# Kernel optimization log

Measured on AMD Instinct MI355X. Metric: run time of the kernel, lower is better.

The kernel has to match this reference:

```python
import jax, jax.numpy as jnp
import numpy as np

N_NODES = 100000
N_EDGES = 1250000
D_FEAT = 64


def setup_inputs() -> dict:
    key = jax.random.key(0)
    kx, ke = jax.random.split(key)
    x = jax.random.normal(kx, (N_NODES, D_FEAT), dtype=jnp.float32)
    edge_index = jax.random.randint(ke, (2, N_EDGES), 0, N_NODES, dtype=jnp.int64)
    return {"x": x, "edge_index": edge_index}


def reference(x, edge_index):
    # propagate: scatter_nested gathers x[idxj] grouped by destination idxi
    # (a ragged per-node neighbor set); the module's sum_nested reduces each
    # group. Expressed densely and jit-ably as gather + segment-sum.
    idxi = edge_index[0, :]  # destination nodes
    idxj = edge_index[1, :]  # source nodes
    messages = x[idxj]  # [E, D] edge-level gather (memory-bound)
    out = jax.ops.segment_sum(messages, idxi, num_segments=N_NODES)  # [N, D]
    return out
```

## Files before the change

kernel.cpp:

```cpp
#include <hip/hip_runtime.h>

#define N_NODES 100000
#define N_EDGES 1250000
#define D_FEAT  64

#define NPB     256
#define NBINS   ((N_NODES + NPB - 1) / NPB)
#define BCAP    4096
#define EPB     4096
#define K1B     ((N_EDGES + EPB - 1) / EPB)
#define OVF_CAP 32768

#define CAP     48


__global__ __launch_bounds__(512) void k1_bin_kernel(
        const int* __restrict__ idxi, const int* __restrict__ idxj,
        int* __restrict__ gcursor, int* __restrict__ ovfcnt,
        int* __restrict__ ovf, int* __restrict__ binbuf) {
    __shared__ int hist[512];
    __shared__ int runstart[512];
    __shared__ int gbase[NBINS];
    __shared__ int cur[NBINS];
    __shared__ int staged[EPB];
    __shared__ unsigned short sbin[EPB];
    int t = threadIdx.x;
    hist[t] = 0;
    __syncthreads();

    long long base = (long long)blockIdx.x * EPB;
    int d[8], s[8], bn[8];
#pragma unroll
    for (int j = 0; j < 8; ++j) {
        long long e = base + t + j * 512;
        if (e < N_EDGES) {
            d[j] = idxi[e];
            s[j] = idxj[e];
            bn[j] = d[j] >> 8;
            atomicAdd(&hist[bn[j]], 1);
        } else {
            bn[j] = -1;
        }
    }
    __syncthreads();

    runstart[t] = hist[t];
    __syncthreads();
    for (int off = 1; off < 512; off <<= 1) {
        int add = (t >= off) ? runstart[t - off] : 0;
        __syncthreads();
        runstart[t] += add;
        __syncthreads();
    }
    int excl = runstart[t] - hist[t];
    __syncthreads();
    runstart[t] = excl;
    if (t < NBINS) {
        gbase[t] = hist[t] ? atomicAdd(&gcursor[t], hist[t]) : 0;
        cur[t] = 0;
    }
    __syncthreads();

#pragma unroll
    for (int j = 0; j < 8; ++j) {
        if (bn[j] >= 0) {
            int lofs = atomicAdd(&cur[bn[j]], 1);
            int idx = runstart[bn[j]] + lofs;
            staged[idx] = ((d[j] & 255) << 17) | s[j];
            sbin[idx] = (unsigned short)bn[j];
        }
    }
    __syncthreads();

    long long rem = (long long)N_EDGES - base;
    int n = (rem < EPB) ? (int)rem : EPB;
    for (int i = t; i < n; i += 512) {
        int b = sbin[i];
        int p = staged[i];
        int tgt = gbase[b] + (i - runstart[b]);
        if (tgt < BCAP) {
            binbuf[(size_t)b * BCAP + tgt] = p;
        } else {
            int op = atomicAdd(ovfcnt, 1);
            if (op < OVF_CAP) { ovf[2 * op] = b * NPB + (p >> 17); ovf[2 * op + 1] = p & 0x1FFFF; }
        }
    }
}

__global__ __launch_bounds__(1024) void k23_fused_kernel(
        const float* __restrict__ x, const int* __restrict__ gcursor,
        const int* __restrict__ binbuf, float* __restrict__ out) {
    __shared__ int cnt[NPB];
    __shared__ int excl[NPB];
    __shared__ int cur[NPB];
    __shared__ int stmp[NPB];
    __shared__ int srt[BCAP];
    int bin = blockIdx.x;
    int t = threadIdx.x;
    if (t < NPB) cnt[t] = 0;
    __syncthreads();

    int n = gcursor[bin];
    if (n > BCAP) n = BCAP;
    const int* src = binbuf + (size_t)bin * BCAP;
    int p[4];
#pragma unroll
    for (int j = 0; j < 4; ++j) {
        int i = t + j * 1024;
        p[j] = (i < n) ? src[i] : -1;
        if (p[j] >= 0) atomicAdd(&cnt[p[j] >> 17], 1);
    }
    __syncthreads();

    if (t < NPB) stmp[t] = cnt[t];
    __syncthreads();
    for (int off = 1; off < NPB; off <<= 1) {
        int v = 0;
        if (t < NPB && t >= off) v = stmp[t - off];
        __syncthreads();
        if (t < NPB) stmp[t] += v;
        __syncthreads();
    }
    if (t < NPB) {
        excl[t] = stmp[t] - cnt[t];
        cur[t] = 0;
    }
    __syncthreads();

#pragma unroll
    for (int j = 0; j < 4; ++j) {
        if (p[j] >= 0) {
            int dl = p[j] >> 17;
            int pos = excl[dl] + atomicAdd(&cur[dl], 1);
            srt[pos] = p[j] & 0x1FFFF;
        }
    }
    __syncthreads();

    int wave = t >> 6;
    int lane = t & 63;
    int sub  = lane >> 4;
    int c4   = lane & 15;
    for (int i = 0; i < 16; ++i) {
        int dloc = wave * 16 + i;
        int node = bin * NPB + dloc;
        if (node >= N_NODES) break;
        int base = excl[dloc];
        int l = cnt[dloc];
        float4 acc = make_float4(0.f, 0.f, 0.f, 0.f);
        int k = 0;
        for (; k + 8 <= l; k += 8) {
            int s0 = srt[base + k + sub];
            int s1 = srt[base + k + 4 + sub];
            const float4 v0 = *(const float4*)(x + (size_t)s0 * D_FEAT + c4 * 4);
            const float4 v1 = *(const float4*)(x + (size_t)s1 * D_FEAT + c4 * 4);
            acc.x += v0.x + v1.x;
            acc.y += v0.y + v1.y;
            acc.z += v0.z + v1.z;
            acc.w += v0.w + v1.w;
        }
        if (k + 4 <= l) {
            int s0 = srt[base + k + sub];
            const float4 v0 = *(const float4*)(x + (size_t)s0 * D_FEAT + c4 * 4);
            acc.x += v0.x; acc.y += v0.y; acc.z += v0.z; acc.w += v0.w;
            k += 4;
        }
        if (k + sub < l) {
            int s0 = srt[base + k + sub];
            const float4 v0 = *(const float4*)(x + (size_t)s0 * D_FEAT + c4 * 4);
            acc.x += v0.x; acc.y += v0.y; acc.z += v0.z; acc.w += v0.w;
        }

        acc.x += __shfl_xor(acc.x, 16, 64);
        acc.y += __shfl_xor(acc.y, 16, 64);
        acc.z += __shfl_xor(acc.z, 16, 64);
        acc.w += __shfl_xor(acc.w, 16, 64);
        acc.x += __shfl_xor(acc.x, 32, 64);
        acc.y += __shfl_xor(acc.y, 32, 64);
        acc.z += __shfl_xor(acc.z, 32, 64);
        acc.w += __shfl_xor(acc.w, 32, 64);

        if (lane < 16) {
            ((float4*)out)[(size_t)node * 16 + c4] = acc;
        }
    }
}

__global__ __launch_bounds__(256) void ovf_fixup_kernel(
        const float* __restrict__ x, const int* __restrict__ ovfcnt,
        const int* __restrict__ ovf, float* __restrict__ out) {
    int n = *ovfcnt;
    if (n > OVF_CAP) n = OVF_CAP;
    long long total = (long long)n * 16;
    long long stride = (long long)gridDim.x * blockDim.x;
    for (long long t = blockIdx.x * blockDim.x + threadIdx.x; t < total; t += stride) {
        int e  = (int)(t >> 4);
        int fo = ((int)t & 15) << 2;
        int d = ovf[2 * e];
        int s = ovf[2 * e + 1];
        const float4 v = *(const float4*)(x + (size_t)s * D_FEAT + fo);
        float* o = out + (size_t)d * D_FEAT + fo;
        atomicAdd(o + 0, v.x);
        atomicAdd(o + 1, v.y);
        atomicAdd(o + 2, v.z);
        atomicAdd(o + 3, v.w);
    }
}


__global__ __launch_bounds__(256) void scatter_pad_kernel(
        const int* __restrict__ idxi, const int* __restrict__ idxj,
        int* __restrict__ cnt, int* __restrict__ ovfcnt,
        int* __restrict__ ovf, int* __restrict__ bucket) {
    int e = blockIdx.x * blockDim.x + threadIdx.x;
    if (e >= N_EDGES) return;
    int d = idxi[e];
    int s = idxj[e];
    int pos = atomicAdd(&cnt[d], 1);
    if (pos < CAP) {
        bucket[(size_t)d * CAP + pos] = s;
    } else {
        int op = atomicAdd(ovfcnt, 1);
        if (op < OVF_CAP) { ovf[2 * op] = d; ovf[2 * op + 1] = s; }
    }
}

__global__ __launch_bounds__(256) void gather_pad_kernel(
        const float* __restrict__ x, const int* __restrict__ cnt,
        const int* __restrict__ bucket, float* __restrict__ out) {
    int node = blockIdx.x * 4 + (threadIdx.x >> 6);
    int lane = threadIdx.x & 63;
    if (node >= N_NODES) return;
    int c = cnt[node];
    if (c > CAP) c = CAP;
    const int* b = bucket + (size_t)node * CAP;
    float acc = 0.f;
    int k = 0;
    for (; k + 4 <= c; k += 4) {
        int4 s4 = *(const int4*)(b + k);
        float a0 = x[(size_t)s4.x * D_FEAT + lane];
        float a1 = x[(size_t)s4.y * D_FEAT + lane];
        float a2 = x[(size_t)s4.z * D_FEAT + lane];
        float a3 = x[(size_t)s4.w * D_FEAT + lane];
        acc += (a0 + a1) + (a2 + a3);
    }
    for (; k < c; ++k) acc += x[(size_t)b[k] * D_FEAT + lane];
    out[(size_t)node * D_FEAT + lane] = acc;
}


__global__ __launch_bounds__(256) void zero_f4_kernel(float* __restrict__ out, int n4) {
    int i = blockIdx.x * blockDim.x + threadIdx.x;
    if (i < n4) ((float4*)out)[i] = make_float4(0.f, 0.f, 0.f, 0.f);
}

__global__ __launch_bounds__(256) void scatter_add_kernel(const float* __restrict__ x,
                                                          const int* __restrict__ idxi,
                                                          const int* __restrict__ idxj,
                                                          float* __restrict__ out) {
    int t = blockIdx.x * blockDim.x + threadIdx.x;
    int e = t >> 4;
    if (e >= N_EDGES) return;
    int fo = (t & 15) << 2;
    int dst = idxi[e];
    int src = idxj[e];
    const float4 v = *(const float4*)(x + (size_t)src * D_FEAT + fo);
    float* o = out + (size_t)dst * D_FEAT + fo;
    atomicAdd(o + 0, v.x);
    atomicAdd(o + 1, v.y);
    atomicAdd(o + 2, v.z);
    atomicAdd(o + 3, v.w);
}

extern "C" void kernel_launch(void* const* d_in, const int* in_sizes, int n_in,
                              void* d_out, int out_size, void* d_ws, size_t ws_size,
                              hipStream_t stream) {
    const float* x  = (const float*)d_in[0];
    const int*   ei = (const int*)d_in[1];
    const int*   idxi = ei;
    const int*   idxj = ei + N_EDGES;
    float* out = (float*)d_out;

    int nbe = (N_EDGES + 255) / 256;
    int gather_blocks = (N_NODES + 3) / 4;

    {
        size_t need = (512 + 16 + 2 * (size_t)OVF_CAP +
                       (size_t)NBINS * BCAP) * sizeof(int);
        if (ws_size >= need) {
            int* gcursor = (int*)d_ws;
            int* ovfcnt  = gcursor + 512;
            int* ovf     = ovfcnt + 16;
            int* binbuf  = ovf + 2 * OVF_CAP;

            hipMemsetAsync(gcursor, 0, (512 + 16) * sizeof(int), stream);
            k1_bin_kernel<<<K1B, 512, 0, stream>>>(idxi, idxj, gcursor, ovfcnt, ovf, binbuf);
            k23_fused_kernel<<<NBINS, 1024, 0, stream>>>(x, gcursor, binbuf, out);
            ovf_fixup_kernel<<<16, 256, 0, stream>>>(x, ovfcnt, ovf, out);
            return;
        }
    }

    {
        size_t need = ((size_t)N_NODES + 16 + 2 * (size_t)OVF_CAP +
                       (size_t)N_NODES * CAP) * sizeof(int);
        if (ws_size >= need) {
            int* cnt    = (int*)d_ws;
            int* ovfcnt = cnt + N_NODES;
            int* ovf    = cnt + N_NODES + 16;
            int* bucket = ovf + 2 * OVF_CAP;

            hipMemsetAsync(cnt, 0, (N_NODES + 16) * sizeof(int), stream);
            scatter_pad_kernel<<<nbe, 256, 0, stream>>>(idxi, idxj, cnt, ovfcnt, ovf, bucket);
            gather_pad_kernel<<<gather_blocks, 256, 0, stream>>>(x, cnt, bucket, out);
            ovf_fixup_kernel<<<16, 256, 0, stream>>>(x, ovfcnt, ovf, out);
            return;
        }
    }

    int n4 = (N_NODES * D_FEAT) / 4;
    zero_f4_kernel<<<(n4 + 255) / 256, 256, 0, stream>>>(out, n4);
    long long total_threads = (long long)N_EDGES * 16;
    scatter_add_kernel<<<(int)((total_threads + 255) / 256), 256, 0, stream>>>(x, idxi, idxj, out);
}
```

Measured before the change: 140.8 us.

## Fuse binning and per-bin gather into one cooperative persistent kernel

Replaces the memset plus three-kernel pipeline (bin, fused sort/gather, overflow fixup) with a single cooperative kernel of 256 blocks of 1024 threads. It zeroes the cursors, bins edges by destination, and after a grid sync sorts each bin locally and gathers with float4 loads plus a wave-level shuffle reduction. Overflow edges are folded in by a linear scan per node instead of a separate atomic kernel. This aims to remove launch and inter-kernel gaps. The costs are grid-sync overhead, lower parallelism (256 blocks walk 391 bins), and a per-node overflow scan that could be expensive if overflow is non-empty.

```diff
diff --git a/kernel.cpp b/kernel.cpp
--- a/kernel.cpp
+++ b/kernel.cpp
@@ -1,4 +1,7 @@
 #include <hip/hip_runtime.h>
+#include <hip/hip_cooperative_groups.h>
+
+namespace cg = cooperative_groups;
 
 #define N_NODES 100000
 #define N_EDGES 1250000
@@ -7,11 +10,216 @@
 #define NPB     256
 #define NBINS   ((N_NODES + NPB - 1) / NPB)
 #define BCAP    4096
+#define GRID    256
+#define EPB_A   ((N_EDGES + GRID - 1) / GRID)
+#define EPAD    4896
+#define OVF_CAP 32768
+
+#define CAP     48
 #define EPB     4096
 #define K1B     ((N_EDGES + EPB - 1) / EPB)
-#define OVF_CAP 32768
-
-#define CAP     48
+
+
+__global__ __launch_bounds__(1024) void mega_kernel(
+        const float* __restrict__ x,
+        const int* __restrict__ idxi, const int* __restrict__ idxj,
+        int* __restrict__ gcursor, int* __restrict__ ovfcnt,
+        int* __restrict__ ovf, int* __restrict__ binbuf,
+        float* __restrict__ out) {
+    __shared__ union {
+        struct {
+            int hist[512];
+            int runstart[512];
+            int gbase[NBINS];
+            int curA[NBINS];
+            int staged[EPAD];
+            unsigned short sbin[EPAD];
+        } a;
+        struct {
+            int cnt[NPB];
+            int excl[NPB];
+            int cur[NPB];
+            int stmp[NPB];
+            int srt[BCAP];
+        } b;
+    } sh;
+
+    cg::grid_group grid = cg::this_grid();
+    int t = threadIdx.x;
+    int gtid = blockIdx.x * 1024 + t;
+
+    if (gtid < NBINS) gcursor[gtid] = 0;
+    if (gtid == NBINS) *ovfcnt = 0;
+    grid.sync();
+
+    int base = blockIdx.x * EPB_A;
+    int end  = base + EPB_A;
+    if (end > N_EDGES) end = N_EDGES;
+
+    if (t < 512) sh.a.hist[t] = 0;
+    __syncthreads();
+
+    int d[5], s[5], bn[5];
+#pragma unroll
+    for (int j = 0; j < 5; ++j) {
+        int e = base + t + j * 1024;
+        if (e < end) {
+            d[j] = idxi[e];
+            s[j] = idxj[e];
+            bn[j] = d[j] >> 8;
+            atomicAdd(&sh.a.hist[bn[j]], 1);
+        } else {
+            bn[j] = -1;
+        }
+    }
+    __syncthreads();
+
+    if (t < 512) sh.a.runstart[t] = sh.a.hist[t];
+    __syncthreads();
+    for (int off = 1; off < 512; off <<= 1) {
+        int add = 0;
+        if (t < 512 && t >= off) add = sh.a.runstart[t - off];
+        __syncthreads();
+        if (t < 512) sh.a.runstart[t] += add;
+        __syncthreads();
+    }
+    int excl = 0;
+    if (t < 512) excl = sh.a.runstart[t] - sh.a.hist[t];
+    __syncthreads();
+    if (t < 512) sh.a.runstart[t] = excl;
+    if (t < NBINS) {
+        sh.a.gbase[t] = sh.a.hist[t] ? atomicAdd(&gcursor[t], sh.a.hist[t]) : 0;
+        sh.a.curA[t] = 0;
+    }
+    __syncthreads();
+
+#pragma unroll
+    for (int j = 0; j < 5; ++j) {
+        if (bn[j] >= 0) {
+            int lofs = atomicAdd(&sh.a.curA[bn[j]], 1);
+            int idx = sh.a.runstart[bn[j]] + lofs;
+            sh.a.staged[idx] = ((d[j] & 255) << 17) | s[j];
+            sh.a.sbin[idx] = (unsigned short)bn[j];
+        }
+    }
+    __syncthreads();
+
+    int n = end - base;
+    for (int i = t; i < n; i += 1024) {
+        int b = sh.a.sbin[i];
+        int p = sh.a.staged[i];
+        int tgt = sh.a.gbase[b] + (i - sh.a.runstart[b]);
+        if (tgt < BCAP) {
+            binbuf[(size_t)b * BCAP + tgt] = p;
+        } else {
+            int op = atomicAdd(ovfcnt, 1);
+            if (op < OVF_CAP) { ovf[2 * op] = b * NPB + (p >> 17); ovf[2 * op + 1] = p & 0x1FFFF; }
+        }
+    }
+
+    grid.sync();
+
+    int novf = *ovfcnt;
+    if (novf > OVF_CAP) novf = OVF_CAP;
+
+    for (int bin = blockIdx.x; bin < NBINS; bin += GRID) {
+        __syncthreads();
+        if (t < NPB) sh.b.cnt[t] = 0;
+        __syncthreads();
+
+        int nb = gcursor[bin];
+        if (nb > BCAP) nb = BCAP;
+        const int* src = binbuf + (size_t)bin * BCAP;
+        int p[4];
+#pragma unroll
+        for (int j = 0; j < 4; ++j) {
+            int i = t + j * 1024;
+            p[j] = (i < nb) ? src[i] : -1;
+            if (p[j] >= 0) atomicAdd(&sh.b.cnt[p[j] >> 17], 1);
+        }
+        __syncthreads();
+
+        if (t < NPB) sh.b.stmp[t] = sh.b.cnt[t];
+        __syncthreads();
+        for (int off = 1; off < NPB; off <<= 1) {
+            int v = 0;
+            if (t < NPB && t >= off) v = sh.b.stmp[t - off];
+            __syncthreads();
+            if (t < NPB) sh.b.stmp[t] += v;
+            __syncthreads();
+        }
+        if (t < NPB) {
+            sh.b.excl[t] = sh.b.stmp[t] - sh.b.cnt[t];
+            sh.b.cur[t] = 0;
+        }
+        __syncthreads();
+
+#pragma unroll
+        for (int j = 0; j < 4; ++j) {
+            if (p[j] >= 0) {
+                int dl = p[j] >> 17;
+                int pos = sh.b.excl[dl] + atomicAdd(&sh.b.cur[dl], 1);
+                sh.b.srt[pos] = p[j] & 0x1FFFF;
+            }
+        }
+        __syncthreads();
+
+        int wave = t >> 6;
+        int lane = t & 63;
+        int sub  = lane >> 4;
+        int c4   = lane & 15;
+        for (int i = 0; i < 16; ++i) {
+            int dloc = wave * 16 + i;
+            int node = bin * NPB + dloc;
+            if (node >= N_NODES) break;
+            int lbase = sh.b.excl[dloc];
+            int l = sh.b.cnt[dloc];
+            float4 acc = make_float4(0.f, 0.f, 0.f, 0.f);
+            int k = 0;
+            for (; k + 8 <= l; k += 8) {
+                int s0 = sh.b.srt[lbase + k + sub];
+                int s1 = sh.b.srt[lbase + k + 4 + sub];
+                const float4 v0 = *(const float4*)(x + (size_t)s0 * D_FEAT + c4 * 4);
+                const float4 v1 = *(const float4*)(x + (size_t)s1 * D_FEAT + c4 * 4);
+                acc.x += v0.x + v1.x;
+                acc.y += v0.y + v1.y;
+                acc.z += v0.z + v1.z;
+                acc.w += v0.w + v1.w;
+            }
+            if (k + 4 <= l) {
+                int s0 = sh.b.srt[lbase + k + sub];
+                const float4 v0 = *(const float4*)(x + (size_t)s0 * D_FEAT + c4 * 4);
+                acc.x += v0.x; acc.y += v0.y; acc.z += v0.z; acc.w += v0.w;
+                k += 4;
+            }
+            if (k + sub < l) {
+                int s0 = sh.b.srt[lbase + k + sub];
+                const float4 v0 = *(const float4*)(x + (size_t)s0 * D_FEAT + c4 * 4);
+                acc.x += v0.x; acc.y += v0.y; acc.z += v0.z; acc.w += v0.w;
+            }
+
+            acc.x += __shfl_xor(acc.x, 16, 64);
+            acc.y += __shfl_xor(acc.y, 16, 64);
+            acc.z += __shfl_xor(acc.z, 16, 64);
+            acc.w += __shfl_xor(acc.w, 16, 64);
+            acc.x += __shfl_xor(acc.x, 32, 64);
+            acc.y += __shfl_xor(acc.y, 32, 64);
+            acc.z += __shfl_xor(acc.z, 32, 64);
+            acc.w += __shfl_xor(acc.w, 32, 64);
+
+            if (lane < 16) {
+                for (int o = 0; o < novf; ++o) {
+                    if (ovf[2 * o] == node) {
+                        int ss = ovf[2 * o + 1];
+                        const float4 vv = *(const float4*)(x + (size_t)ss * D_FEAT + c4 * 4);
+                        acc.x += vv.x; acc.y += vv.y; acc.z += vv.z; acc.w += vv.w;
+                    }
+                }
+                ((float4*)out)[(size_t)node * 16 + c4] = acc;
+            }
+        }
+    }
+}
 
 
 __global__ __launch_bounds__(512) void k1_bin_kernel(
@@ -208,47 +416,6 @@
 }
 
 
-__global__ __launch_bounds__(256) void scatter_pad_kernel(
-        const int* __restrict__ idxi, const int* __restrict__ idxj,
-        int* __restrict__ cnt, int* __restrict__ ovfcnt,
-        int* __restrict__ ovf, int* __restrict__ bucket) {
-    int e = blockIdx.x * blockDim.x + threadIdx.x;
-    if (e >= N_EDGES) return;
-    int d = idxi[e];
-    int s = idxj[e];
-    int pos = atomicAdd(&cnt[d], 1);
-    if (pos < CAP) {
-        bucket[(size_t)d * CAP + pos] = s;
-    } else {
-        int op = atomicAdd(ovfcnt, 1);
-        if (op < OVF_CAP) { ovf[2 * op] = d; ovf[2 * op + 1] = s; }
-    }
-}
-
-__global__ __launch_bounds__(256) void gather_pad_kernel(
-        const float* __restrict__ x, const int* __restrict__ cnt,
-        const int* __restrict__ bucket, float* __restrict__ out) {
-    int node = blockIdx.x * 4 + (threadIdx.x >> 6);
-    int lane = threadIdx.x & 63;
-    if (node >= N_NODES) return;
-    int c = cnt[node];
-    if (c > CAP) c = CAP;
-    const int* b = bucket + (size_t)node * CAP;
-    float acc = 0.f;
-    int k = 0;
-    for (; k + 4 <= c; k += 4) {
-        int4 s4 = *(const int4*)(b + k);
-        float a0 = x[(size_t)s4.x * D_FEAT + lane];
-        float a1 = x[(size_t)s4.y * D_FEAT + lane];
-        float a2 = x[(size_t)s4.z * D_FEAT + lane];
-        float a3 = x[(size_t)s4.w * D_FEAT + lane];
-        acc += (a0 + a1) + (a2 + a3);
-    }
-    for (; k < c; ++k) acc += x[(size_t)b[k] * D_FEAT + lane];
-    out[(size_t)node * D_FEAT + lane] = acc;
-}
-
-
 __global__ __launch_bounds__(256) void zero_f4_kernel(float* __restrict__ out, int n4) {
     int i = blockIdx.x * blockDim.x + threadIdx.x;
     if (i < n4) ((float4*)out)[i] = make_float4(0.f, 0.f, 0.f, 0.f);
@@ -281,41 +448,26 @@
     const int*   idxj = ei + N_EDGES;
     float* out = (float*)d_out;
 
-    int nbe = (N_EDGES + 255) / 256;
-    int gather_blocks = (N_NODES + 3) / 4;
-
-    {
-        size_t need = (512 + 16 + 2 * (size_t)OVF_CAP +
-                       (size_t)NBINS * BCAP) * sizeof(int);
-        if (ws_size >= need) {
-            int* gcursor = (int*)d_ws;
-            int* ovfcnt  = gcursor + 512;
-            int* ovf     = ovfcnt + 16;
-            int* binbuf  = ovf + 2 * OVF_CAP;
-
-            hipMemsetAsync(gcursor, 0, (512 + 16) * sizeof(int), stream);
-            k1_bin_kernel<<<K1B, 512, 0, stream>>>(idxi, idxj, gcursor, ovfcnt, ovf, binbuf);
-            k23_fused_kernel<<<NBINS, 1024, 0, stream>>>(x, gcursor, binbuf, out);
-            ovf_fixup_kernel<<<16, 256, 0, stream>>>(x, ovfcnt, ovf, out);
-            return;
-        }
-    }
-
-    {
-        size_t need = ((size_t)N_NODES + 16 + 2 * (size_t)OVF_CAP +
-                       (size_t)N_NODES * CAP) * sizeof(int);
-        if (ws_size >= need) {
-            int* cnt    = (int*)d_ws;
-            int* ovfcnt = cnt + N_NODES;
-            int* ovf    = cnt + N_NODES + 16;
-            int* bucket = ovf + 2 * OVF_CAP;
-
-            hipMemsetAsync(cnt, 0, (N_NODES + 16) * sizeof(int), stream);
-            scatter_pad_kernel<<<nbe, 256, 0, stream>>>(idxi, idxj, cnt, ovfcnt, ovf, bucket);
-            gather_pad_kernel<<<gather_blocks, 256, 0, stream>>>(x, cnt, bucket, out);
-            ovf_fixup_kernel<<<16, 256, 0, stream>>>(x, ovfcnt, ovf, out);
-            return;
-        }
+    size_t need = (512 + 16 + 2 * (size_t)OVF_CAP +
+                   (size_t)NBINS * BCAP) * sizeof(int);
+    if (ws_size >= need) {
+        int* gcursor = (int*)d_ws;
+        int* ovfcnt  = gcursor + 512;
+        int* ovf     = ovfcnt + 16;
+        int* binbuf  = ovf + 2 * OVF_CAP;
+
+        void* args[] = { (void*)&x, (void*)&idxi, (void*)&idxj,
+                         (void*)&gcursor, (void*)&ovfcnt, (void*)&ovf,
+                         (void*)&binbuf, (void*)&out };
+        hipError_t err = hipLaunchCooperativeKernel(
+            (const void*)mega_kernel, dim3(GRID), dim3(1024), args, 0, stream);
+        if (err == hipSuccess) return;
+
+        hipMemsetAsync(gcursor, 0, (512 + 16) * sizeof(int), stream);
+        k1_bin_kernel<<<K1B, 512, 0, stream>>>(idxi, idxj, gcursor, ovfcnt, ovf, binbuf);
+        k23_fused_kernel<<<NBINS, 1024, 0, stream>>>(x, gcursor, binbuf, out);
+        ovf_fixup_kernel<<<16, 256, 0, stream>>>(x, ovfcnt, ovf, out);
+        return;
     }
 
     int n4 = (N_NODES * D_FEAT) / 4;
```

Measured after the change: 207.4 us. 47.3% more time.

## Gather from fp16 copy of node features in fused bin kernel

Applied to the files above, without the earlier changes.

Adds a conversion kernel that writes x as fp16 into the workspace, and a variant of the fused sort-and-gather kernel that reads fp16 rows with ushort4 loads and accumulates in fp32. Four edges are processed in parallel per wave, with shuffle reductions across 16-lane groups. The goal is to halve the bytes of the random row gathers, which dominate the kernel, at the cost of an extra pass over x and reduced input precision. The padded-bucket fallback path is removed.

```diff
diff --git a/kernel.cpp b/kernel.cpp
--- a/kernel.cpp
+++ b/kernel.cpp
@@ -1,4 +1,5 @@
 #include <hip/hip_runtime.h>
+#include <hip/hip_fp16.h>
 
 #define N_NODES 100000
 #define N_EDGES 1250000
@@ -11,8 +12,19 @@
 #define K1B     ((N_EDGES + EPB - 1) / EPB)
 #define OVF_CAP 32768
 
-#define CAP     48
-
+
+__global__ __launch_bounds__(256) void cvt_kernel(const float* __restrict__ x,
+                                                  unsigned short* __restrict__ xh) {
+    int i = blockIdx.x * 256 + threadIdx.x;
+    if (i >= N_NODES * D_FEAT / 4) return;
+    const float4 v = ((const float4*)x)[i];
+    ushort4 h;
+    h.x = __half_as_ushort(__float2half_rn(v.x));
+    h.y = __half_as_ushort(__float2half_rn(v.y));
+    h.z = __half_as_ushort(__float2half_rn(v.z));
+    h.w = __half_as_ushort(__float2half_rn(v.w));
+    ((ushort4*)xh)[i] = h;
+}
 
 __global__ __launch_bounds__(512) void k1_bin_kernel(
         const int* __restrict__ idxi, const int* __restrict__ idxj,
@@ -83,6 +95,111 @@
         } else {
             int op = atomicAdd(ovfcnt, 1);
             if (op < OVF_CAP) { ovf[2 * op] = b * NPB + (p >> 17); ovf[2 * op + 1] = p & 0x1FFFF; }
+        }
+    }
+}
+
+__global__ __launch_bounds__(1024) void k23_fused_h_kernel(
+        const unsigned short* __restrict__ xh, const int* __restrict__ gcursor,
+        const int* __restrict__ binbuf, float* __restrict__ out) {
+    __shared__ int cnt[NPB];
+    __shared__ int excl[NPB];
+    __shared__ int cur[NPB];
+    __shared__ int stmp[NPB];
+    __shared__ int srt[BCAP];
+    int bin = blockIdx.x;
+    int t = threadIdx.x;
+    if (t < NPB) cnt[t] = 0;
+    __syncthreads();
+
+    int n = gcursor[bin];
+    if (n > BCAP) n = BCAP;
+    const int* src = binbuf + (size_t)bin * BCAP;
+    int p[4];
+#pragma unroll
+    for (int j = 0; j < 4; ++j) {
+        int i = t + j * 1024;
+        p[j] = (i < n) ? src[i] : -1;
+        if (p[j] >= 0) atomicAdd(&cnt[p[j] >> 17], 1);
+    }
+    __syncthreads();
+
+    if (t < NPB) stmp[t] = cnt[t];
+    __syncthreads();
+    for (int off = 1; off < NPB; off <<= 1) {
+        int v = 0;
+        if (t < NPB && t >= off) v = stmp[t - off];
+        __syncthreads();
+        if (t < NPB) stmp[t] += v;
+        __syncthreads();
+    }
+    if (t < NPB) {
+        excl[t] = stmp[t] - cnt[t];
+        cur[t] = 0;
+    }
+    __syncthreads();
+
+#pragma unroll
+    for (int j = 0; j < 4; ++j) {
+        if (p[j] >= 0) {
+            int dl = p[j] >> 17;
+            int pos = excl[dl] + atomicAdd(&cur[dl], 1);
+            srt[pos] = p[j] & 0x1FFFF;
+        }
+    }
+    __syncthreads();
+
+    int wave = t >> 6;
+    int lane = t & 63;
+    int sub  = lane >> 4;
+    int c4   = lane & 15;
+    for (int i = 0; i < 16; ++i) {
+        int dloc = wave * 16 + i;
+        int node = bin * NPB + dloc;
+        if (node >= N_NODES) break;
+        int base = excl[dloc];
+        int l = cnt[dloc];
+        float4 acc = make_float4(0.f, 0.f, 0.f, 0.f);
+        int k = 0;
+        for (; k + 8 <= l; k += 8) {
+            int s0 = srt[base + k + sub];
+            int s1 = srt[base + k + 4 + sub];
+            ushort4 r0 = ((const ushort4*)(xh + (size_t)s0 * D_FEAT))[c4];
+            ushort4 r1 = ((const ushort4*)(xh + (size_t)s1 * D_FEAT))[c4];
+            acc.x += __half2float(__ushort_as_half(r0.x)) + __half2float(__ushort_as_half(r1.x));
+            acc.y += __half2float(__ushort_as_half(r0.y)) + __half2float(__ushort_as_half(r1.y));
+            acc.z += __half2float(__ushort_as_half(r0.z)) + __half2float(__ushort_as_half(r1.z));
+            acc.w += __half2float(__ushort_as_half(r0.w)) + __half2float(__ushort_as_half(r1.w));
+        }
+        if (k + 4 <= l) {
+            int s0 = srt[base + k + sub];
+            ushort4 r0 = ((const ushort4*)(xh + (size_t)s0 * D_FEAT))[c4];
+            acc.x += __half2float(__ushort_as_half(r0.x));
+            acc.y += __half2float(__ushort_as_half(r0.y));
+            acc.z += __half2float(__ushort_as_half(r0.z));
+            acc.w += __half2float(__ushort_as_half(r0.w));
+            k += 4;
+        }
+        if (k + sub < l) {
+            int s0 = srt[base + k + sub];
+            ushort4 r0 = ((const ushort4*)(xh + (size_t)s0 * D_FEAT))[c4];
+            acc.x += __half2float(__ushort_as_half(r0.x));
+            acc.y += __half2float(__ushort_as_half(r0.y));
+            acc.z += __half2float(__ushort_as_half(r0.z));
+            acc.w += __half2float(__ushort_as_half(r0.w));
+        }
+
+        acc.x += __shfl_xor(acc.x, 16, 64);
+        acc.y += __shfl_xor(acc.y, 16, 64);
+        acc.z += __shfl_xor(acc.z, 16, 64);
+        acc.w += __shfl_xor(acc.w, 16, 64);
+        acc.x += __shfl_xor(acc.x, 32, 64);
+        acc.y += __shfl_xor(acc.y, 32, 64);
+        acc.z += __shfl_xor(acc.z, 32, 64);
+        acc.w += __shfl_xor(acc.w, 32, 64);
+
+        if (lane < 16) {
+            ((float4*)out)[(size_t)node * 16 + c4] = acc;
         }
     }
 }
@@ -208,47 +325,6 @@
 }
 
 
-__global__ __launch_bounds__(256) void scatter_pad_kernel(
-        const int* __restrict__ idxi, const int* __restrict__ idxj,
-        int* __restrict__ cnt, int* __restrict__ ovfcnt,
-        int* __restrict__ ovf, int* __restrict__ bucket) {
-    int e = blockIdx.x * blockDim.x + threadIdx.x;
-    if (e >= N_EDGES) return;
-    int d = idxi[e];
-    int s = idxj[e];
-    int pos = atomicAdd(&cnt[d], 1);
-    if (pos < CAP) {
-        bucket[(size_t)d * CAP + pos] = s;
-    } else {
-        int op = atomicAdd(ovfcnt, 1);
-        if (op < OVF_CAP) { ovf[2 * op] = d; ovf[2 * op + 1] = s; }
-    }
-}
-
-__global__ __launch_bounds__(256) void gather_pad_kernel(
-        const float* __restrict__ x, const int* __restrict__ cnt,
-        const int* __restrict__ bucket, float* __restrict__ out) {
-    int node = blockIdx.x * 4 + (threadIdx.x >> 6);
-    int lane = threadIdx.x & 63;
-    if (node >= N_NODES) return;
-    int c = cnt[node];
-    if (c > CAP) c = CAP;
-    const int* b = bucket + (size_t)node * CAP;
-    float acc = 0.f;
-    int k = 0;
-    for (; k + 4 <= c; k += 4) {
-        int4 s4 = *(const int4*)(b + k);
-        float a0 = x[(size_t)s4.x * D_FEAT + lane];
-        float a1 = x[(size_t)s4.y * D_FEAT + lane];
-        float a2 = x[(size_t)s4.z * D_FEAT + lane];
-        float a3 = x[(size_t)s4.w * D_FEAT + lane];
-        acc += (a0 + a1) + (a2 + a3);
-    }
-    for (; k < c; ++k) acc += x[(size_t)b[k] * D_FEAT + lane];
-    out[(size_t)node * D_FEAT + lane] = acc;
-}
-
-
 __global__ __launch_bounds__(256) void zero_f4_kernel(float* __restrict__ out, int n4) {
     int i = blockIdx.x * blockDim.x + threadIdx.x;
     if (i < n4) ((float4*)out)[i] = make_float4(0.f, 0.f, 0.f, 0.f);
@@ -281,41 +357,30 @@
     const int*   idxj = ei + N_EDGES;
     float* out = (float*)d_out;
 
-    int nbe = (N_EDGES + 255) / 256;
-    int gather_blocks = (N_NODES + 3) / 4;
-
-    {
-        size_t need = (512 + 16 + 2 * (size_t)OVF_CAP +
-                       (size_t)NBINS * BCAP) * sizeof(int);
-        if (ws_size >= need) {
-            int* gcursor = (int*)d_ws;
-            int* ovfcnt  = gcursor + 512;
-            int* ovf     = ovfcnt + 16;
-            int* binbuf  = ovf + 2 * OVF_CAP;
-
-            hipMemsetAsync(gcursor, 0, (512 + 16) * sizeof(int), stream);
-            k1_bin_kernel<<<K1B, 512, 0, stream>>>(idxi, idxj, gcursor, ovfcnt, ovf, binbuf);
+    size_t base_ints = 512 + 16 + 2 * (size_t)OVF_CAP + (size_t)NBINS * BCAP;
+    size_t xh_ints   = (size_t)N_NODES * D_FEAT / 2;
+    size_t need_h    = (base_ints + xh_ints) * sizeof(int);
+    size_t need_f    = base_ints * sizeof(int);
+
+    if (ws_size >= need_f) {
+        int* gcursor = (int*)d_ws;
+        int* ovfcnt  = gcursor + 512;
+        int* ovf     = ovfcnt + 16;
+        int* binbuf  = ovf + 2 * OVF_CAP;
+
+        hipMemsetAsync(gcursor, 0, (512 + 16) * sizeof(int), stream);
+        k1_bin_kernel<<<K1B, 512, 0, stream>>>(idxi, idxj, gcursor, ovfcnt, ovf, binbuf);
+
+        if (ws_size >= need_h) {
+            unsigned short* xh = (unsigned short*)(binbuf + (size_t)NBINS * BCAP);
+            int n4 = N_NODES * D_FEAT / 4;
+            cvt_kernel<<<(n4 + 255) / 256, 256, 0, stream>>>(x, xh);
+            k23_fused_h_kernel<<<NBINS, 1024, 0, stream>>>(xh, gcursor, binbuf, out);
+        } else {
             k23_fused_kernel<<<NBINS, 1024, 0, stream>>>(x, gcursor, binbuf, out);
-            ovf_fixup_kernel<<<16, 256, 0, stream>>>(x, ovfcnt, ovf, out);
-            return;
-        }
-    }
-
-    {
-        size_t need = ((size_t)N_NODES + 16 + 2 * (size_t)OVF_CAP +
-                       (size_t)N_NODES * CAP) * sizeof(int);
-        if (ws_size >= need) {
-            int* cnt    = (int*)d_ws;
-            int* ovfcnt = cnt + N_NODES;
-            int* ovf    = cnt + N_NODES + 16;
-            int* bucket = ovf + 2 * OVF_CAP;
-
-            hipMemsetAsync(cnt, 0, (N_NODES + 16) * sizeof(int), stream);
-            scatter_pad_kernel<<<nbe, 256, 0, stream>>>(idxi, idxj, cnt, ovfcnt, ovf, bucket);
-            gather_pad_kernel<<<gather_blocks, 256, 0, stream>>>(x, cnt, bucket, out);
-            ovf_fixup_kernel<<<16, 256, 0, stream>>>(x, ovfcnt, ovf, out);
-            return;
-        }
+        }
+        ovf_fixup_kernel<<<16, 256, 0, stream>>>(x, ovfcnt, ovf, out);
+        return;
     }
 
     int n4 = (N_NODES * D_FEAT) / 4;
```

Measured after the change: 143.2 us. Within noise of the previous version (+1.7%).
